# Kernel tuning notes

Hardware: AMD Instinct MI355X
Metric: run time of the kernel (lower is better)

## Reference

```python
import jax, jax.numpy as jnp
import numpy as np

V, E_DIM, H, B, T = 390, 256, 512, 64, 512
START = 388


def setup_inputs() -> dict:
    key = jax.random.key(0)
    ks = jax.random.split(key, 32)
    s = 0.05
    rn = lambda k, shape: jax.random.normal(k, shape, jnp.float32) * s
    inp = {
        "input": jax.random.normal(ks[0], (B, T, V), jnp.float32),
        # encoder params
        "enc_emb": rn(ks[1], (V, E_DIM)),
        "enc_Wih0": rn(ks[2], (3 * H, E_DIM)),
        "enc_Whh0": rn(ks[3], (3 * H, H)),
        "enc_bih0": rn(ks[4], (3 * H,)),
        "enc_bhh0": rn(ks[5], (3 * H,)),
        "enc_Wih1": rn(ks[6], (3 * H, H)),
        "enc_Whh1": rn(ks[7], (3 * H, H)),
        "enc_bih1": rn(ks[8], (3 * H,)),
        "enc_bhh1": rn(ks[9], (3 * H,)),
        # decoder params
        "dec_emb": rn(ks[10], (V, E_DIM)),
        "dec_Wih0": rn(ks[11], (3 * H, E_DIM)),
        "dec_Whh0": rn(ks[12], (3 * H, H)),
        "dec_bih0": rn(ks[13], (3 * H,)),
        "dec_bhh0": rn(ks[14], (3 * H,)),
        "dec_Wih1": rn(ks[15], (3 * H, H)),
        "dec_Whh1": rn(ks[16], (3 * H, H)),
        "dec_bih1": rn(ks[17], (3 * H,)),
        "dec_bhh1": rn(ks[18], (3 * H,)),
        # prediction head
        "Wp1": rn(ks[19], (H, H)),
        "bp1": rn(ks[20], (H,)),
        "Wp2": rn(ks[21], (V, H)),
        "bp2": rn(ks[22], (V,)),
    }
    return inp


def _gru_cell(x, h, Wih, Whh, bih, bhh):
    # PyTorch GRU cell: gates ordered (r, z, n)
    gi = x @ Wih.T + bih
    gh = h @ Whh.T + bhh
    ir, iz, inn = jnp.split(gi, 3, axis=-1)
    hr, hz, hn = jnp.split(gh, 3, axis=-1)
    r = jax.nn.sigmoid(ir + hr)
    z = jax.nn.sigmoid(iz + hz)
    n = jnp.tanh(inn + r * hn)
    return (1.0 - z) * n + z * h


def reference(input, enc_emb, enc_Wih0, enc_Whh0, enc_bih0, enc_bhh0,
              enc_Wih1, enc_Whh1, enc_bih1, enc_bhh1,
              dec_emb, dec_Wih0, dec_Whh0, dec_bih0, dec_bhh0,
              dec_Wih1, dec_Whh1, dec_bih1, dec_bhh1,
              Wp1, bp1, Wp2, bp2):
    batch, max_len, vocab = input.shape
    hdim = enc_Whh0.shape[1]

    # ---- Encoder: soft embedding + 2-layer GRU, keep final hidden states ----
    x = jnp.einsum('btv,ve->bte', input, enc_emb)  # [B,T,E]
    xt = jnp.transpose(x, (1, 0, 2))               # time-major [T,B,E]
    h0 = jnp.zeros((batch, hdim), input.dtype)

    def step0(h, xt_):
        h = _gru_cell(xt_, h, enc_Wih0, enc_Whh0, enc_bih0, enc_bhh0)
        return h, h
    h1_enc, seq1 = jax.lax.scan(step0, h0, xt)

    def step1(h, xt_):
        h = _gru_cell(xt_, h, enc_Wih1, enc_Whh1, enc_bih1, enc_bhh1)
        return h, None
    h2_enc, _ = jax.lax.scan(step1, h0, seq1)

    tok0 = jnp.full((batch,), START, jnp.int32)
    rng0 = jax.random.key(42)

    def dec_step(carry, _):
        h1, h2, tok, rng = carry
        rng, sk = jax.random.split(rng)
        xe = dec_emb[tok]                               # [B,E]
        h1 = _gru_cell(xe, h1, dec_Wih0, dec_Whh0, dec_bih0, dec_bhh0)
        h2 = _gru_cell(h1, h2, dec_Wih1, dec_Whh1, dec_bih1, dec_bhh1)
        hid = h2 @ Wp1.T + bp1
        hid = jnp.where(hid >= 0, hid, 0.1 * hid)       # LeakyReLU(0.1)
        logits = hid @ Wp2.T + bp2                      # temp=1 -> logits/temp == logits
        probs = jax.nn.softmax(logits, axis=-1)
        tok = jax.random.categorical(sk, logits, axis=-1).astype(jnp.int32)
        return (h1, h2, tok, rng), (probs, tok)

    _, (probs_seq, toks) = jax.lax.scan(
        dec_step, (h1_enc, h2_enc, tok0, rng0), None, length=max_len - 1)

    start_oh = jax.nn.one_hot(tok0, vocab, dtype=input.dtype)  # [B,V]
    outputs = jnp.concatenate(
        [start_oh[:, None, :], jnp.transpose(probs_seq, (1, 0, 2))], axis=1)
    max_output = jnp.concatenate(
        [jnp.full((batch, 1), float(START), jnp.float32),
         toks.T.astype(jnp.float32)], axis=1)
    return outputs, max_output
```

## Files before the change

### kernel.cpp

```cpp
#include <hip/hip_runtime.h>
#include <math.h>


#define BB 64
#define TT 512
#define VV 390
#define EE 256
#define HH 512

static __device__ __forceinline__ void tf2x32(unsigned k0, unsigned k1,
                                              unsigned x0, unsigned x1,
                                              unsigned &o0, unsigned &o1) {
  unsigned ks2 = k0 ^ k1 ^ 0x1BD11BDAu;
  x0 += k0; x1 += k1;
#define TFR(r) x0 += x1; x1 = (x1 << (r)) | (x1 >> (32 - (r))); x1 ^= x0;
  TFR(13) TFR(15) TFR(26) TFR(6)
  x0 += k1; x1 += ks2 + 1u;
  TFR(17) TFR(29) TFR(16) TFR(24)
  x0 += ks2; x1 += k0 + 2u;
  TFR(13) TFR(15) TFR(26) TFR(6)
  x0 += k0; x1 += k1 + 3u;
  TFR(17) TFR(29) TFR(16) TFR(24)
  x0 += k1; x1 += ks2 + 4u;
  TFR(13) TFR(15) TFR(26) TFR(6)
  x0 += ks2; x1 += k0 + 5u;
#undef TFR
  o0 = x0; o1 = x1;
}

static __device__ __forceinline__ float sigm(float x) {
  return 1.0f / (1.0f + expf(-x));
}

template <int K>
static __device__ __forceinline__ void dot3_kb(const float* __restrict__ X, int b,
    const float* __restrict__ w0, const float* __restrict__ w1,
    const float* __restrict__ w2, float &r0, float &r1, float &r2) {
  const float4* q0 = (const float4*)w0;
  const float4* q1 = (const float4*)w1;
  const float4* q2 = (const float4*)w2;
  float s0 = 0.f, s1 = 0.f, s2 = 0.f;
#pragma unroll 4
  for (int k4 = 0; k4 < (K >> 2); ++k4) {
    float4 u0 = q0[k4], u1 = q1[k4], u2 = q2[k4];
    int kb = (k4 << 8) + b;
    float x0 = X[kb], x1 = X[kb + 64], x2 = X[kb + 128], x3 = X[kb + 192];
    s0 = fmaf(x0, u0.x, s0); s0 = fmaf(x1, u0.y, s0); s0 = fmaf(x2, u0.z, s0); s0 = fmaf(x3, u0.w, s0);
    s1 = fmaf(x0, u1.x, s1); s1 = fmaf(x1, u1.y, s1); s1 = fmaf(x2, u1.z, s1); s1 = fmaf(x3, u1.w, s1);
    s2 = fmaf(x0, u2.x, s2); s2 = fmaf(x1, u2.y, s2); s2 = fmaf(x2, u2.z, s2); s2 = fmaf(x3, u2.w, s2);
  }
  r0 = s0; r1 = s1; r2 = s2;
}

template <int K>
static __device__ __forceinline__ void dot3_row(const float* __restrict__ xrow,
    const float* __restrict__ w0, const float* __restrict__ w1,
    const float* __restrict__ w2, float &r0, float &r1, float &r2) {
  const float4* xq = (const float4*)xrow;
  const float4* q0 = (const float4*)w0;
  const float4* q1 = (const float4*)w1;
  const float4* q2 = (const float4*)w2;
  float s0 = 0.f, s1 = 0.f, s2 = 0.f;
#pragma unroll 4
  for (int k4 = 0; k4 < (K >> 2); ++k4) {
    float4 x = xq[k4];
    float4 u0 = q0[k4], u1 = q1[k4], u2 = q2[k4];
    s0 = fmaf(x.x, u0.x, s0); s0 = fmaf(x.y, u0.y, s0); s0 = fmaf(x.z, u0.z, s0); s0 = fmaf(x.w, u0.w, s0);
    s1 = fmaf(x.x, u1.x, s1); s1 = fmaf(x.y, u1.y, s1); s1 = fmaf(x.z, u1.z, s1); s1 = fmaf(x.w, u1.w, s1);
    s2 = fmaf(x.x, u2.x, s2); s2 = fmaf(x.y, u2.y, s2); s2 = fmaf(x.z, u2.z, s2); s2 = fmaf(x.w, u2.w, s2);
  }
  r0 = s0; r1 = s1; r2 = s2;
}

__global__ __launch_bounds__(256) void k_init(float* __restrict__ out,
    float* __restrict__ h1buf, float* __restrict__ h2buf,
    int* __restrict__ tok, unsigned* __restrict__ rng) {
  int wg = blockIdx.x, tid = threadIdx.x;
  for (int i = wg * 256 + tid; i < HH * BB; i += 64 * 256) {
    h1buf[i] = 0.f;
    h2buf[i] = 0.f;
  }
  for (int v = tid; v < VV; v += 256)
    out[(size_t)wg * TT * VV + v] = (v == 388) ? 1.0f : 0.0f;
  if (tid == 0) {
    out[(size_t)BB * TT * VV + (size_t)wg * TT] = 388.0f;
    tok[wg] = 388;
    if (wg == 0) { rng[0] = 0u; rng[1] = 42u; rng[2] = 0u; rng[3] = 0u; }
  }
}

__global__ __launch_bounds__(256) void k_xgemm(const float* __restrict__ input,
    const float* __restrict__ emb, float* __restrict__ xT) {
  int t = blockIdx.x, tid = threadIdx.x;
  int s = tid >> 6, b = tid & 63;
  __shared__ float lin[64 * 65];
  float4 acc[16];
#pragma unroll
  for (int i = 0; i < 16; ++i) acc[i] = make_float4(0.f, 0.f, 0.f, 0.f);
  for (int k0 = 0; k0 < VV; k0 += 64) {
    int kmax = min(64, VV - k0);
    __syncthreads();
#pragma unroll
    for (int r = 0; r < 16; ++r) {
      int idx = r * 256 + tid;
      int b2 = idx >> 6, kk = idx & 63;
      if (kk < kmax)
        lin[kk * 65 + b2] = input[((size_t)b2 * TT + t) * VV + k0 + kk];
    }
    __syncthreads();
    for (int kk = 0; kk < kmax; ++kk) {
      float xv = lin[kk * 65 + b];
      const float4* er = (const float4*)(emb + (size_t)(k0 + kk) * EE);
#pragma unroll
      for (int i = 0; i < 16; ++i) {
        float4 w = er[s + 4 * i];
        acc[i].x = fmaf(xv, w.x, acc[i].x);
        acc[i].y = fmaf(xv, w.y, acc[i].y);
        acc[i].z = fmaf(xv, w.z, acc[i].z);
        acc[i].w = fmaf(xv, w.w, acc[i].w);
      }
    }
  }
  float* dst0 = xT + (size_t)t * (EE * 64);
#pragma unroll
  for (int i = 0; i < 16; ++i) {
    int e = (s + 4 * i) * 4;
    float* d = dst0 + e * 64 + b;
    d[0] = acc[i].x; d[64] = acc[i].y; d[128] = acc[i].z; d[192] = acc[i].w;
  }
}

__global__ __launch_bounds__(256) void k_enc_step(int t,
    const float* __restrict__ xT, float* __restrict__ h1buf, float* __restrict__ h2buf,
    const float* __restrict__ Wih0, const float* __restrict__ Whh0,
    const float* __restrict__ bih0, const float* __restrict__ bhh0,
    const float* __restrict__ Wih1, const float* __restrict__ Whh1,
    const float* __restrict__ bih1, const float* __restrict__ bhh1) {
  int wg = blockIdx.x, tid = threadIdx.x;
  int s = tid >> 6, b = tid & 63;
  const float* h1_r = h1buf + (t & 1) * (HH * BB);
  float* h1_w = h1buf + ((t + 1) & 1) * (HH * BB);
  if (wg < 128) {
    if (t >= TT) return;
    int j = wg * 4 + s;
    float ar, az, an, hr, hz, hn;
    dot3_kb<EE>(xT + (size_t)t * (EE * 64), b,
                Wih0 + (size_t)j * EE, Wih0 + (size_t)(512 + j) * EE,
                Wih0 + (size_t)(1024 + j) * EE, ar, az, an);
    dot3_kb<HH>(h1_r, b,
                Whh0 + (size_t)j * HH, Whh0 + (size_t)(512 + j) * HH,
                Whh0 + (size_t)(1024 + j) * HH, hr, hz, hn);
    float r = sigm((ar + bih0[j]) + (hr + bhh0[j]));
    float z = sigm((az + bih0[512 + j]) + (hz + bhh0[512 + j]));
    float n = tanhf((an + bih0[1024 + j]) + r * (hn + bhh0[1024 + j]));
    h1_w[j * 64 + b] = (1.0f - z) * n + z * h1_r[j * 64 + b];
  } else {
    if (t < 1) return;
    int j = (wg - 128) * 4 + s;
    const float* h2_r = h2buf + ((t + 1) & 1) * (HH * BB);
    float* h2_w = h2buf + (t & 1) * (HH * BB);
    float ar, az, an, hr, hz, hn;
    dot3_kb<HH>(h1_r, b,
                Wih1 + (size_t)j * HH, Wih1 + (size_t)(512 + j) * HH,
                Wih1 + (size_t)(1024 + j) * HH, ar, az, an);
    dot3_kb<HH>(h2_r, b,
                Whh1 + (size_t)j * HH, Whh1 + (size_t)(512 + j) * HH,
                Whh1 + (size_t)(1024 + j) * HH, hr, hz, hn);
    float r = sigm((ar + bih1[j]) + (hr + bhh1[j]));
    float z = sigm((az + bih1[512 + j]) + (hz + bhh1[512 + j]));
    float n = tanhf((an + bih1[1024 + j]) + r * (hn + bhh1[1024 + j]));
    h2_w[j * 64 + b] = (1.0f - z) * n + z * h2_r[j * 64 + b];
  }
}

__global__ __launch_bounds__(256) void k_decA(int d, float* __restrict__ h1buf,
    const float* __restrict__ demb, const float* __restrict__ Wih,
    const float* __restrict__ Whh, const float* __restrict__ bih,
    const float* __restrict__ bhh, const int* __restrict__ tok) {
  int wg = blockIdx.x, tid = threadIdx.x, s = tid >> 6, b = tid & 63;
  const float* h1_r = h1buf + (d & 1) * (HH * BB);
  float* h1_w = h1buf + ((d + 1) & 1) * (HH * BB);
  int j = wg * 4 + s;
  int tk = tok[b];
  float ar, az, an, hr, hz, hn;
  dot3_row<EE>(demb + (size_t)tk * EE,
               Wih + (size_t)j * EE, Wih + (size_t)(512 + j) * EE,
               Wih + (size_t)(1024 + j) * EE, ar, az, an);
  dot3_kb<HH>(h1_r, b,
              Whh + (size_t)j * HH, Whh + (size_t)(512 + j) * HH,
              Whh + (size_t)(1024 + j) * HH, hr, hz, hn);
  float r = sigm((ar + bih[j]) + (hr + bhh[j]));
  float z = sigm((az + bih[512 + j]) + (hz + bhh[512 + j]));
  float n = tanhf((an + bih[1024 + j]) + r * (hn + bhh[1024 + j]));
  h1_w[j * 64 + b] = (1.0f - z) * n + z * h1_r[j * 64 + b];
}

__global__ __launch_bounds__(256) void k_decB(int d, const float* __restrict__ h1buf,
    float* __restrict__ h2buf, const float* __restrict__ Wih,
    const float* __restrict__ Whh, const float* __restrict__ bih,
    const float* __restrict__ bhh) {
  int wg = blockIdx.x, tid = threadIdx.x, s = tid >> 6, b = tid & 63;
  const float* h1n = h1buf + ((d + 1) & 1) * (HH * BB);
  const float* h2r = h2buf + (d & 1) * (HH * BB);
  float* h2w = h2buf + ((d + 1) & 1) * (HH * BB);
  int j = wg * 4 + s;
  float ar, az, an, hr, hz, hn;
  dot3_kb<HH>(h1n, b,
              Wih + (size_t)j * HH, Wih + (size_t)(512 + j) * HH,
              Wih + (size_t)(1024 + j) * HH, ar, az, an);
  dot3_kb<HH>(h2r, b,
              Whh + (size_t)j * HH, Whh + (size_t)(512 + j) * HH,
              Whh + (size_t)(1024 + j) * HH, hr, hz, hn);
  float r = sigm((ar + bih[j]) + (hr + bhh[j]));
  float z = sigm((az + bih[512 + j]) + (hz + bhh[512 + j]));
  float n = tanhf((an + bih[1024 + j]) + r * (hn + bhh[1024 + j]));
  h2w[j * 64 + b] = (1.0f - z) * n + z * h2r[j * 64 + b];
}

__global__ __launch_bounds__(256) void k_decC(int d, const float* __restrict__ h2buf,
    const float* __restrict__ Wp1, const float* __restrict__ bp1,
    const float* __restrict__ Wp2, const float* __restrict__ bp2,
    float* __restrict__ out, int* __restrict__ tok, unsigned* __restrict__ rng) {
  __shared__ __align__(16) float lh[HH];
  __shared__ __align__(16) float lhid[HH];
  __shared__ float lv[VV];
  __shared__ float rf[8];
  __shared__ int ri[4];
  int b = blockIdx.x, tid = threadIdx.x;
  const float* h2 = h2buf + ((d + 1) & 1) * (HH * BB);
  lh[tid] = h2[tid * 64 + b];
  lh[tid + 256] = h2[(tid + 256) * 64 + b];
  __syncthreads();
  for (int c = tid; c < HH; c += 256) {
    const float4* w = (const float4*)(Wp1 + (size_t)c * HH);
    float a = 0.f;
#pragma unroll 4
    for (int k4 = 0; k4 < HH / 4; ++k4) {
      float4 q = w[k4];
      float4 hv = *(const float4*)&lh[k4 * 4];
      a = fmaf(hv.x, q.x, a); a = fmaf(hv.y, q.y, a);
      a = fmaf(hv.z, q.z, a); a = fmaf(hv.w, q.w, a);
    }
    a += bp1[c];
    lhid[c] = (a >= 0.f) ? a : 0.1f * a;
  }
  __syncthreads();
  for (int c = tid; c < VV; c += 256) {
    const float4* w = (const float4*)(Wp2 + (size_t)c * HH);
    float a = 0.f;
#pragma unroll 4
    for (int k4 = 0; k4 < HH / 4; ++k4) {
      float4 q = w[k4];
      float4 hv = *(const float4*)&lhid[k4 * 4];
      a = fmaf(hv.x, q.x, a); a = fmaf(hv.y, q.y, a);
      a = fmaf(hv.z, q.z, a); a = fmaf(hv.w, q.w, a);
    }
    lv[c] = a + bp2[c];
  }
  __syncthreads();
  float m = -INFINITY;
  for (int c = tid; c < VV; c += 256) m = fmaxf(m, lv[c]);
  for (int off = 32; off > 0; off >>= 1) m = fmaxf(m, __shfl_down(m, off, 64));
  if ((tid & 63) == 0) rf[tid >> 6] = m;
  __syncthreads();
  if (tid == 0) rf[4] = fmaxf(fmaxf(rf[0], rf[1]), fmaxf(rf[2], rf[3]));
  __syncthreads();
  m = rf[4];
  unsigned k0r = rng[(d & 1) * 2], k1r = rng[(d & 1) * 2 + 1];
  unsigned sk0, sk1;
  tf2x32(k0r, k1r, 0u, 1u, sk0, sk1);
  float by = -INFINITY; int bc = 0x7fffffff;
  for (int c = tid; c < VV; c += 256) {
    unsigned o0, o1;
    tf2x32(sk0, sk1, 0u, (unsigned)(b * VV + c), o0, o1);
    unsigned bits = o0 ^ o1;
    float f = __uint_as_float(0x3f800000u | (bits >> 9)) - 1.0f;
    float u = (f > 0.f) ? f : 1.17549435e-38f;
    float g = (float)(-log(-log((double)u)));
    float y = lv[c] + g;
    if (y > by || (y == by && c < bc)) { by = y; bc = c; }
  }
  for (int off = 32; off > 0; off >>= 1) {
    float oy = __shfl_down(by, off, 64);
    int oc = __shfl_down(bc, off, 64);
    if (oy > by || (oy == by && oc < bc)) { by = oy; bc = oc; }
  }
  if ((tid & 63) == 0) { rf[tid >> 6] = by; ri[tid >> 6] = bc; }
  __syncthreads();
  if (tid == 0) {
    by = rf[0]; bc = ri[0];
    for (int w2 = 1; w2 < 4; ++w2)
      if (rf[w2] > by || (rf[w2] == by && ri[w2] < bc)) { by = rf[w2]; bc = ri[w2]; }
    tok[b] = bc;
    out[(size_t)BB * TT * VV + (size_t)b * TT + (d + 1)] = (float)bc;
    if (b == 0) {
      unsigned n0, n1;
      tf2x32(k0r, k1r, 0u, 0u, n0, n1);
      rng[((d + 1) & 1) * 2] = n0;
      rng[((d + 1) & 1) * 2 + 1] = n1;
    }
  }
  __syncthreads();
  float e0 = 0.f, e1 = 0.f, ssum = 0.f;
  {
    int c = tid;
    if (c < VV) { e0 = expf(lv[c] - m); ssum += e0; }
    c = tid + 256;
    if (c < VV) { e1 = expf(lv[c] - m); ssum += e1; }
  }
  for (int off = 32; off > 0; off >>= 1) ssum += __shfl_down(ssum, off, 64);
  if ((tid & 63) == 0) rf[tid >> 6] = ssum;
  __syncthreads();
  if (tid == 0) rf[4] = (rf[0] + rf[1]) + (rf[2] + rf[3]);
  __syncthreads();
  float S = rf[4];
  float* orow = out + ((size_t)b * TT + (d + 1)) * VV;
  if (tid < VV) orow[tid] = e0 / S;
  if (tid + 256 < VV) orow[tid + 256] = e1 / S;
}

extern "C" void kernel_launch(void* const* d_in, const int* in_sizes, int n_in,
                              void* d_out, int out_size, void* d_ws, size_t ws_size,
                              hipStream_t stream) {
  (void)in_sizes; (void)n_in; (void)out_size; (void)ws_size;
  const float* input = (const float*)d_in[0];
  const float* e_emb = (const float*)d_in[1];
  const float* eWih0 = (const float*)d_in[2];
  const float* eWhh0 = (const float*)d_in[3];
  const float* ebih0 = (const float*)d_in[4];
  const float* ebhh0 = (const float*)d_in[5];
  const float* eWih1 = (const float*)d_in[6];
  const float* eWhh1 = (const float*)d_in[7];
  const float* ebih1 = (const float*)d_in[8];
  const float* ebhh1 = (const float*)d_in[9];
  const float* d_emb = (const float*)d_in[10];
  const float* dWih0 = (const float*)d_in[11];
  const float* dWhh0 = (const float*)d_in[12];
  const float* dbih0 = (const float*)d_in[13];
  const float* dbhh0 = (const float*)d_in[14];
  const float* dWih1 = (const float*)d_in[15];
  const float* dWhh1 = (const float*)d_in[16];
  const float* dbih1 = (const float*)d_in[17];
  const float* dbhh1 = (const float*)d_in[18];
  const float* Wp1   = (const float*)d_in[19];
  const float* bp1   = (const float*)d_in[20];
  const float* Wp2   = (const float*)d_in[21];
  const float* bp2   = (const float*)d_in[22];
  float* out = (float*)d_out;

  float* xT = (float*)d_ws;
  float* h1buf = xT + (size_t)TT * EE * 64;
  float* h2buf = h1buf + 2 * HH * BB;
  int* tok = (int*)(h2buf + 2 * HH * BB);
  unsigned* rng = (unsigned*)(tok + 64);

  k_init<<<64, 256, 0, stream>>>(out, h1buf, h2buf, tok, rng);
  k_xgemm<<<TT, 256, 0, stream>>>(input, e_emb, xT);
  for (int t = 0; t <= TT; ++t)
    k_enc_step<<<256, 256, 0, stream>>>(t, xT, h1buf, h2buf,
        eWih0, eWhh0, ebih0, ebhh0, eWih1, eWhh1, ebih1, ebhh1);
  for (int d = 0; d < TT - 1; ++d) {
    k_decA<<<128, 256, 0, stream>>>(d, h1buf, d_emb, dWih0, dWhh0, dbih0, dbhh0, tok);
    k_decB<<<128, 256, 0, stream>>>(d, h1buf, h2buf, dWih1, dWhh1, dbih1, dbhh1);
    k_decC<<<64, 256, 0, stream>>>(d, h2buf, Wp1, bp1, Wp2, bp2, out, tok, rng);
  }
}
```

Baseline: 86.14 ms.

## Replace per-step kernel launches with persistent kernels using grid barriers

```diff
diff --git a/kernel.cpp b/kernel.cpp
--- a/kernel.cpp
+++ b/kernel.cpp
@@ -72,9 +72,27 @@
   r0 = s0; r1 = s1; r2 = s2;
 }
 
-__global__ __launch_bounds__(256) void k_init(float* __restrict__ out,
-    float* __restrict__ h1buf, float* __restrict__ h2buf,
-    int* __restrict__ tok, unsigned* __restrict__ rng) {
+static __device__ __forceinline__ void gridbar(unsigned* bar, unsigned nwg) {
+  __syncthreads();
+  if (threadIdx.x == 0) {
+    unsigned v = __hip_atomic_fetch_add(bar, 1u, __ATOMIC_ACQ_REL,
+                                        __HIP_MEMORY_SCOPE_AGENT);
+    unsigned gen = v >> 16;
+    if ((v & 0xffffu) == nwg - 1u) {
+      __hip_atomic_store(bar, (gen + 1u) << 16, __ATOMIC_RELEASE,
+                         __HIP_MEMORY_SCOPE_AGENT);
+    } else {
+      while ((__hip_atomic_load(bar, __ATOMIC_RELAXED,
+                                __HIP_MEMORY_SCOPE_AGENT) >> 16) == gen)
+        __builtin_amdgcn_s_sleep(1);
+      __builtin_amdgcn_fence(__ATOMIC_ACQUIRE, "agent");
+    }
+  }
+  __syncthreads();
+}
+
+__global__ __launch_bounds__(256) void k_init(float* out,
+    float* h1buf, float* h2buf, int* tok, unsigned* rng, unsigned* ebar) {
   int wg = blockIdx.x, tid = threadIdx.x;
   for (int i = wg * 256 + tid; i < HH * BB; i += 64 * 256) {
     h1buf[i] = 0.f;
@@ -85,7 +103,10 @@
   if (tid == 0) {
     out[(size_t)BB * TT * VV + (size_t)wg * TT] = 388.0f;
     tok[wg] = 388;
-    if (wg == 0) { rng[0] = 0u; rng[1] = 42u; rng[2] = 0u; rng[3] = 0u; }
+    if (wg == 0) {
+      rng[0] = 0u; rng[1] = 42u; rng[2] = 0u; rng[3] = 0u;
+      ebar[0] = 0u;
+    }
   }
 }
 
@@ -130,193 +151,205 @@
   }
 }
 
-__global__ __launch_bounds__(256) void k_enc_step(int t,
-    const float* __restrict__ xT, float* __restrict__ h1buf, float* __restrict__ h2buf,
+__global__ __launch_bounds__(256) void k_enc_persist(
+    const float* __restrict__ xT, float* h1buf, float* h2buf,
     const float* __restrict__ Wih0, const float* __restrict__ Whh0,
     const float* __restrict__ bih0, const float* __restrict__ bhh0,
     const float* __restrict__ Wih1, const float* __restrict__ Whh1,
-    const float* __restrict__ bih1, const float* __restrict__ bhh1) {
+    const float* __restrict__ bih1, const float* __restrict__ bhh1,
+    unsigned* ebar, unsigned* dbar) {
   int wg = blockIdx.x, tid = threadIdx.x;
   int s = tid >> 6, b = tid & 63;
-  const float* h1_r = h1buf + (t & 1) * (HH * BB);
-  float* h1_w = h1buf + ((t + 1) & 1) * (HH * BB);
-  if (wg < 128) {
-    if (t >= TT) return;
-    int j = wg * 4 + s;
-    float ar, az, an, hr, hz, hn;
-    dot3_kb<EE>(xT + (size_t)t * (EE * 64), b,
-                Wih0 + (size_t)j * EE, Wih0 + (size_t)(512 + j) * EE,
-                Wih0 + (size_t)(1024 + j) * EE, ar, az, an);
-    dot3_kb<HH>(h1_r, b,
-                Whh0 + (size_t)j * HH, Whh0 + (size_t)(512 + j) * HH,
-                Whh0 + (size_t)(1024 + j) * HH, hr, hz, hn);
-    float r = sigm((ar + bih0[j]) + (hr + bhh0[j]));
-    float z = sigm((az + bih0[512 + j]) + (hz + bhh0[512 + j]));
-    float n = tanhf((an + bih0[1024 + j]) + r * (hn + bhh0[1024 + j]));
-    h1_w[j * 64 + b] = (1.0f - z) * n + z * h1_r[j * 64 + b];
-  } else {
-    if (t < 1) return;
-    int j = (wg - 128) * 4 + s;
-    const float* h2_r = h2buf + ((t + 1) & 1) * (HH * BB);
-    float* h2_w = h2buf + (t & 1) * (HH * BB);
-    float ar, az, an, hr, hz, hn;
-    dot3_kb<HH>(h1_r, b,
-                Wih1 + (size_t)j * HH, Wih1 + (size_t)(512 + j) * HH,
-                Wih1 + (size_t)(1024 + j) * HH, ar, az, an);
-    dot3_kb<HH>(h2_r, b,
-                Whh1 + (size_t)j * HH, Whh1 + (size_t)(512 + j) * HH,
-                Whh1 + (size_t)(1024 + j) * HH, hr, hz, hn);
-    float r = sigm((ar + bih1[j]) + (hr + bhh1[j]));
-    float z = sigm((az + bih1[512 + j]) + (hz + bhh1[512 + j]));
-    float n = tanhf((an + bih1[1024 + j]) + r * (hn + bhh1[1024 + j]));
-    h2_w[j * 64 + b] = (1.0f - z) * n + z * h2_r[j * 64 + b];
-  }
-}
-
-__global__ __launch_bounds__(256) void k_decA(int d, float* __restrict__ h1buf,
-    const float* __restrict__ demb, const float* __restrict__ Wih,
-    const float* __restrict__ Whh, const float* __restrict__ bih,
-    const float* __restrict__ bhh, const int* __restrict__ tok) {
-  int wg = blockIdx.x, tid = threadIdx.x, s = tid >> 6, b = tid & 63;
-  const float* h1_r = h1buf + (d & 1) * (HH * BB);
-  float* h1_w = h1buf + ((d + 1) & 1) * (HH * BB);
-  int j = wg * 4 + s;
-  int tk = tok[b];
-  float ar, az, an, hr, hz, hn;
-  dot3_row<EE>(demb + (size_t)tk * EE,
-               Wih + (size_t)j * EE, Wih + (size_t)(512 + j) * EE,
-               Wih + (size_t)(1024 + j) * EE, ar, az, an);
-  dot3_kb<HH>(h1_r, b,
-              Whh + (size_t)j * HH, Whh + (size_t)(512 + j) * HH,
-              Whh + (size_t)(1024 + j) * HH, hr, hz, hn);
-  float r = sigm((ar + bih[j]) + (hr + bhh[j]));
-  float z = sigm((az + bih[512 + j]) + (hz + bhh[512 + j]));
-  float n = tanhf((an + bih[1024 + j]) + r * (hn + bhh[1024 + j]));
-  h1_w[j * 64 + b] = (1.0f - z) * n + z * h1_r[j * 64 + b];
-}
-
-__global__ __launch_bounds__(256) void k_decB(int d, const float* __restrict__ h1buf,
-    float* __restrict__ h2buf, const float* __restrict__ Wih,
-    const float* __restrict__ Whh, const float* __restrict__ bih,
-    const float* __restrict__ bhh) {
-  int wg = blockIdx.x, tid = threadIdx.x, s = tid >> 6, b = tid & 63;
-  const float* h1n = h1buf + ((d + 1) & 1) * (HH * BB);
-  const float* h2r = h2buf + (d & 1) * (HH * BB);
-  float* h2w = h2buf + ((d + 1) & 1) * (HH * BB);
-  int j = wg * 4 + s;
-  float ar, az, an, hr, hz, hn;
-  dot3_kb<HH>(h1n, b,
-              Wih + (size_t)j * HH, Wih + (size_t)(512 + j) * HH,
-              Wih + (size_t)(1024 + j) * HH, ar, az, an);
-  dot3_kb<HH>(h2r, b,
-              Whh + (size_t)j * HH, Whh + (size_t)(512 + j) * HH,
-              Whh + (size_t)(1024 + j) * HH, hr, hz, hn);
-  float r = sigm((ar + bih[j]) + (hr + bhh[j]));
-  float z = sigm((az + bih[512 + j]) + (hz + bhh[512 + j]));
-  float n = tanhf((an + bih[1024 + j]) + r * (hn + bhh[1024 + j]));
-  h2w[j * 64 + b] = (1.0f - z) * n + z * h2r[j * 64 + b];
-}
-
-__global__ __launch_bounds__(256) void k_decC(int d, const float* __restrict__ h2buf,
+  for (int t = 0; t <= TT; ++t) {
+    const float* h1_r = h1buf + (t & 1) * (HH * BB);
+    float* h1_w = h1buf + ((t + 1) & 1) * (HH * BB);
+    if (wg < 128) {
+      if (t < TT) {
+        int j = wg * 4 + s;
+        float ar, az, an, hr, hz, hn;
+        dot3_kb<EE>(xT + (size_t)t * (EE * 64), b,
+                    Wih0 + (size_t)j * EE, Wih0 + (size_t)(512 + j) * EE,
+                    Wih0 + (size_t)(1024 + j) * EE, ar, az, an);
+        dot3_kb<HH>(h1_r, b,
+                    Whh0 + (size_t)j * HH, Whh0 + (size_t)(512 + j) * HH,
+                    Whh0 + (size_t)(1024 + j) * HH, hr, hz, hn);
+        float r = sigm((ar + bih0[j]) + (hr + bhh0[j]));
+        float z = sigm((az + bih0[512 + j]) + (hz + bhh0[512 + j]));
+        float n = tanhf((an + bih0[1024 + j]) + r * (hn + bhh0[1024 + j]));
+        h1_w[j * 64 + b] = (1.0f - z) * n + z * h1_r[j * 64 + b];
+      }
+    } else {
+      if (t >= 1) {
+        int j = (wg - 128) * 4 + s;
+        const float* h2_r = h2buf + ((t + 1) & 1) * (HH * BB);
+        float* h2_w = h2buf + (t & 1) * (HH * BB);
+        float ar, az, an, hr, hz, hn;
+        dot3_kb<HH>(h1_r, b,
+                    Wih1 + (size_t)j * HH, Wih1 + (size_t)(512 + j) * HH,
+                    Wih1 + (size_t)(1024 + j) * HH, ar, az, an);
+        dot3_kb<HH>(h2_r, b,
+                    Whh1 + (size_t)j * HH, Whh1 + (size_t)(512 + j) * HH,
+                    Whh1 + (size_t)(1024 + j) * HH, hr, hz, hn);
+        float r = sigm((ar + bih1[j]) + (hr + bhh1[j]));
+        float z = sigm((az + bih1[512 + j]) + (hz + bhh1[512 + j]));
+        float n = tanhf((an + bih1[1024 + j]) + r * (hn + bhh1[1024 + j]));
+        h2_w[j * 64 + b] = (1.0f - z) * n + z * h2_r[j * 64 + b];
+      }
+    }
+    if (t == TT && wg == 0 && tid == 0) dbar[0] = 0u;
+    gridbar(ebar, 256u);
+  }
+}
+
+__global__ __launch_bounds__(256) void k_dec_persist(
+    float* h1buf, float* h2buf,
+    const float* __restrict__ demb,
+    const float* __restrict__ dWih0, const float* __restrict__ dWhh0,
+    const float* __restrict__ dbih0, const float* __restrict__ dbhh0,
+    const float* __restrict__ dWih1, const float* __restrict__ dWhh1,
+    const float* __restrict__ dbih1, const float* __restrict__ dbhh1,
     const float* __restrict__ Wp1, const float* __restrict__ bp1,
     const float* __restrict__ Wp2, const float* __restrict__ bp2,
-    float* __restrict__ out, int* __restrict__ tok, unsigned* __restrict__ rng) {
+    float* out, int* tok, unsigned* rng, unsigned* dbar) {
+  int wg = blockIdx.x, tid = threadIdx.x;
+  int s = tid >> 6, b = tid & 63;
   __shared__ __align__(16) float lh[HH];
   __shared__ __align__(16) float lhid[HH];
   __shared__ float lv[VV];
   __shared__ float rf[8];
   __shared__ int ri[4];
-  int b = blockIdx.x, tid = threadIdx.x;
-  const float* h2 = h2buf + ((d + 1) & 1) * (HH * BB);
-  lh[tid] = h2[tid * 64 + b];
-  lh[tid + 256] = h2[(tid + 256) * 64 + b];
-  __syncthreads();
-  for (int c = tid; c < HH; c += 256) {
-    const float4* w = (const float4*)(Wp1 + (size_t)c * HH);
-    float a = 0.f;
+  for (int d = 0; d < TT - 1; ++d) {
+    {
+      const float* h1_r = h1buf + (d & 1) * (HH * BB);
+      float* h1_w = h1buf + ((d + 1) & 1) * (HH * BB);
+      int j = wg * 4 + s;
+      int tk = tok[b];
+      float ar, az, an, hr, hz, hn;
+      dot3_row<EE>(demb + (size_t)tk * EE,
+                   dWih0 + (size_t)j * EE, dWih0 + (size_t)(512 + j) * EE,
+                   dWih0 + (size_t)(1024 + j) * EE, ar, az, an);
+      dot3_kb<HH>(h1_r, b,
+                  dWhh0 + (size_t)j * HH, dWhh0 + (size_t)(512 + j) * HH,
+                  dWhh0 + (size_t)(1024 + j) * HH, hr, hz, hn);
+      float r = sigm((ar + dbih0[j]) + (hr + dbhh0[j]));
+      float z = sigm((az + dbih0[512 + j]) + (hz + dbhh0[512 + j]));
+      float n = tanhf((an + dbih0[1024 + j]) + r * (hn + dbhh0[1024 + j]));
+      h1_w[j * 64 + b] = (1.0f - z) * n + z * h1_r[j * 64 + b];
+    }
+    gridbar(dbar, 128u);
+    {
+      const float* h1n = h1buf + ((d + 1) & 1) * (HH * BB);
+      const float* h2r = h2buf + (d & 1) * (HH * BB);
+      float* h2w = h2buf + ((d + 1) & 1) * (HH * BB);
+      int j = wg * 4 + s;
+      float ar, az, an, hr, hz, hn;
+      dot3_kb<HH>(h1n, b,
+                  dWih1 + (size_t)j * HH, dWih1 + (size_t)(512 + j) * HH,
+                  dWih1 + (size_t)(1024 + j) * HH, ar, az, an);
+      dot3_kb<HH>(h2r, b,
+                  dWhh1 + (size_t)j * HH, dWhh1 + (size_t)(512 + j) * HH,
+                  dWhh1 + (size_t)(1024 + j) * HH, hr, hz, hn);
+      float r = sigm((ar + dbih1[j]) + (hr + dbhh1[j]));
+      float z = sigm((az + dbih1[512 + j]) + (hz + dbhh1[512 + j]));
+      float n = tanhf((an + dbih1[1024 + j]) + r * (hn + dbhh1[1024 + j]));
+      h2w[j * 64 + b] = (1.0f - z) * n + z * h2r[j * 64 + b];
+    }
+    gridbar(dbar, 128u);
+    if (wg < 64) {
+      int brow = wg;
+      const float* h2 = h2buf + ((d + 1) & 1) * (HH * BB);
+      lh[tid] = h2[tid * 64 + brow];
+      lh[tid + 256] = h2[(tid + 256) * 64 + brow];
+      __syncthreads();
+      for (int c = tid; c < HH; c += 256) {
+        const float4* w = (const float4*)(Wp1 + (size_t)c * HH);
+        float a = 0.f;
 #pragma unroll 4
-    for (int k4 = 0; k4 < HH / 4; ++k4) {
-      float4 q = w[k4];
-      float4 hv = *(const float4*)&lh[k4 * 4];
-      a = fmaf(hv.x, q.x, a); a = fmaf(hv.y, q.y, a);
-      a = fmaf(hv.z, q.z, a); a = fmaf(hv.w, q.w, a);
-    }
-    a += bp1[c];
-    lhid[c] = (a >= 0.f) ? a : 0.1f * a;
-  }
-  __syncthreads();
-  for (int c = tid; c < VV; c += 256) {
-    const float4* w = (const float4*)(Wp2 + (size_t)c * HH);
-    float a = 0.f;
+        for (int k4 = 0; k4 < HH / 4; ++k4) {
+          float4 q = w[k4];
+          float4 hv = *(const float4*)&lh[k4 * 4];
+          a = fmaf(hv.x, q.x, a); a = fmaf(hv.y, q.y, a);
+          a = fmaf(hv.z, q.z, a); a = fmaf(hv.w, q.w, a);
+        }
+        a += bp1[c];
+        lhid[c] = (a >= 0.f) ? a : 0.1f * a;
+      }
+      __syncthreads();
+      for (int c = tid; c < VV; c += 256) {
+        const float4* w = (const float4*)(Wp2 + (size_t)c * HH);
+        float a = 0.f;
 #pragma unroll 4
-    for (int k4 = 0; k4 < HH / 4; ++k4) {
-      float4 q = w[k4];
-      float4 hv = *(const float4*)&lhid[k4 * 4];
-      a = fmaf(hv.x, q.x, a); a = fmaf(hv.y, q.y, a);
-      a = fmaf(hv.z, q.z, a); a = fmaf(hv.w, q.w, a);
-    }
-    lv[c] = a + bp2[c];
-  }
-  __syncthreads();
-  float m = -INFINITY;
-  for (int c = tid; c < VV; c += 256) m = fmaxf(m, lv[c]);
-  for (int off = 32; off > 0; off >>= 1) m = fmaxf(m, __shfl_down(m, off, 64));
-  if ((tid & 63) == 0) rf[tid >> 6] = m;
-  __syncthreads();
-  if (tid == 0) rf[4] = fmaxf(fmaxf(rf[0], rf[1]), fmaxf(rf[2], rf[3]));
-  __syncthreads();
-  m = rf[4];
-  unsigned k0r = rng[(d & 1) * 2], k1r = rng[(d & 1) * 2 + 1];
-  unsigned sk0, sk1;
-  tf2x32(k0r, k1r, 0u, 1u, sk0, sk1);
-  float by = -INFINITY; int bc = 0x7fffffff;
-  for (int c = tid; c < VV; c += 256) {
-    unsigned o0, o1;
-    tf2x32(sk0, sk1, 0u, (unsigned)(b * VV + c), o0, o1);
-    unsigned bits = o0 ^ o1;
-    float f = __uint_as_float(0x3f800000u | (bits >> 9)) - 1.0f;
-    float u = (f > 0.f) ? f : 1.17549435e-38f;
-    float g = (float)(-log(-log((double)u)));
-    float y = lv[c] + g;
-    if (y > by || (y == by && c < bc)) { by = y; bc = c; }
-  }
-  for (int off = 32; off > 0; off >>= 1) {
-    float oy = __shfl_down(by, off, 64);
-    int oc = __shfl_down(bc, off, 64);
-    if (oy > by || (oy == by && oc < bc)) { by = oy; bc = oc; }
-  }
-  if ((tid & 63) == 0) { rf[tid >> 6] = by; ri[tid >> 6] = bc; }
-  __syncthreads();
-  if (tid == 0) {
-    by = rf[0]; bc = ri[0];
-    for (int w2 = 1; w2 < 4; ++w2)
-      if (rf[w2] > by || (rf[w2] == by && ri[w2] < bc)) { by = rf[w2]; bc = ri[w2]; }
-    tok[b] = bc;
-    out[(size_t)BB * TT * VV + (size_t)b * TT + (d + 1)] = (float)bc;
-    if (b == 0) {
-      unsigned n0, n1;
-      tf2x32(k0r, k1r, 0u, 0u, n0, n1);
-      rng[((d + 1) & 1) * 2] = n0;
-      rng[((d + 1) & 1) * 2 + 1] = n1;
-    }
-  }
-  __syncthreads();
-  float e0 = 0.f, e1 = 0.f, ssum = 0.f;
-  {
-    int c = tid;
-    if (c < VV) { e0 = expf(lv[c] - m); ssum += e0; }
-    c = tid + 256;
-    if (c < VV) { e1 = expf(lv[c] - m); ssum += e1; }
-  }
-  for (int off = 32; off > 0; off >>= 1) ssum += __shfl_down(ssum, off, 64);
-  if ((tid & 63) == 0) rf[tid >> 6] = ssum;
-  __syncthreads();
-  if (tid == 0) rf[4] = (rf[0] + rf[1]) + (rf[2] + rf[3]);
-  __syncthreads();
-  float S = rf[4];
-  float* orow = out + ((size_t)b * TT + (d + 1)) * VV;
-  if (tid < VV) orow[tid] = e0 / S;
-  if (tid + 256 < VV) orow[tid + 256] = e1 / S;
+        for (int k4 = 0; k4 < HH / 4; ++k4) {
+          float4 q = w[k4];
+          float4 hv = *(const float4*)&lhid[k4 * 4];
+          a = fmaf(hv.x, q.x, a); a = fmaf(hv.y, q.y, a);
+          a = fmaf(hv.z, q.z, a); a = fmaf(hv.w, q.w, a);
+        }
+        lv[c] = a + bp2[c];
+      }
+      __syncthreads();
+      float m = -INFINITY;
+      for (int c = tid; c < VV; c += 256) m = fmaxf(m, lv[c]);
+      for (int off = 32; off > 0; off >>= 1) m = fmaxf(m, __shfl_down(m, off, 64));
+      if ((tid & 63) == 0) rf[tid >> 6] = m;
+      __syncthreads();
+      if (tid == 0) rf[4] = fmaxf(fmaxf(rf[0], rf[1]), fmaxf(rf[2], rf[3]));
+      __syncthreads();
+      m = rf[4];
+      unsigned k0r = rng[(d & 1) * 2], k1r = rng[(d & 1) * 2 + 1];
+      unsigned sk0, sk1;
+      tf2x32(k0r, k1r, 0u, 1u, sk0, sk1);
+      float by = -INFINITY; int bc = 0x7fffffff;
+      for (int c = tid; c < VV; c += 256) {
+        unsigned o0, o1;
+        tf2x32(sk0, sk1, 0u, (unsigned)(brow * VV + c), o0, o1);
+        unsigned bits = o0 ^ o1;
+        float f = __uint_as_float(0x3f800000u | (bits >> 9)) - 1.0f;
+        float u = (f > 0.f) ? f : 1.17549435e-38f;
+        float g = (float)(-log(-log((double)u)));
+        float y = lv[c] + g;
+        if (y > by || (y == by && c < bc)) { by = y; bc = c; }
+      }
+      for (int off = 32; off > 0; off >>= 1) {
+        float oy = __shfl_down(by, off, 64);
+        int oc = __shfl_down(bc, off, 64);
+        if (oy > by || (oy == by && oc < bc)) { by = oy; bc = oc; }
+      }
+      if ((tid & 63) == 0) { rf[tid >> 6] = by; ri[tid >> 6] = bc; }
+      __syncthreads();
+      if (tid == 0) {
+        by = rf[0]; bc = ri[0];
+        for (int w2 = 1; w2 < 4; ++w2)
+          if (rf[w2] > by || (rf[w2] == by && ri[w2] < bc)) { by = rf[w2]; bc = ri[w2]; }
+        tok[brow] = bc;
+        out[(size_t)BB * TT * VV + (size_t)brow * TT + (d + 1)] = (float)bc;
+        if (brow == 0) {
+          unsigned n0, n1;
+          tf2x32(k0r, k1r, 0u, 0u, n0, n1);
+          rng[((d + 1) & 1) * 2] = n0;
+          rng[((d + 1) & 1) * 2 + 1] = n1;
+        }
+      }
+      __syncthreads();
+      float e0 = 0.f, e1 = 0.f, ssum = 0.f;
+      {
+        int c = tid;
+        if (c < VV) { e0 = expf(lv[c] - m); ssum += e0; }
+        c = tid + 256;
+        if (c < VV) { e1 = expf(lv[c] - m); ssum += e1; }
+      }
+      for (int off = 32; off > 0; off >>= 1) ssum += __shfl_down(ssum, off, 64);
+      if ((tid & 63) == 0) rf[tid >> 6] = ssum;
+      __syncthreads();
+      if (tid == 0) rf[4] = (rf[0] + rf[1]) + (rf[2] + rf[3]);
+      __syncthreads();
+      float S = rf[4];
+      float* orow = out + ((size_t)brow * TT + (d + 1)) * VV;
+      if (tid < VV) orow[tid] = e0 / S;
+      if (tid + 256 < VV) orow[tid + 256] = e1 / S;
+    }
+    gridbar(dbar, 128u);
+  }
 }
 
 extern "C" void kernel_launch(void* const* d_in, const int* in_sizes, int n_in,
@@ -353,15 +386,14 @@
   float* h2buf = h1buf + 2 * HH * BB;
   int* tok = (int*)(h2buf + 2 * HH * BB);
   unsigned* rng = (unsigned*)(tok + 64);
-
-  k_init<<<64, 256, 0, stream>>>(out, h1buf, h2buf, tok, rng);
+  unsigned* ebar = (unsigned*)(out + VV);
+  unsigned* dbar = (unsigned*)xT;
+
+  k_init<<<64, 256, 0, stream>>>(out, h1buf, h2buf, tok, rng, ebar);
   k_xgemm<<<TT, 256, 0, stream>>>(input, e_emb, xT);
-  for (int t = 0; t <= TT; ++t)
-    k_enc_step<<<256, 256, 0, stream>>>(t, xT, h1buf, h2buf,
-        eWih0, eWhh0, ebih0, ebhh0, eWih1, eWhh1, ebih1, ebhh1);
-  for (int d = 0; d < TT - 1; ++d) {
-    k_decA<<<128, 256, 0, stream>>>(d, h1buf, d_emb, dWih0, dWhh0, dbih0, dbhh0, tok);
-    k_decB<<<128, 256, 0, stream>>>(d, h1buf, h2buf, dWih1, dWhh1, dbih1, dbhh1);
-    k_decC<<<64, 256, 0, stream>>>(d, h2buf, Wp1, bp1, Wp2, bp2, out, tok, rng);
-  }
-}
+  k_enc_persist<<<256, 256, 0, stream>>>(xT, h1buf, h2buf,
+      eWih0, eWhh0, ebih0, ebhh0, eWih1, eWhh1, ebih1, ebhh1, ebar, dbar);
+  k_dec_persist<<<128, 256, 0, stream>>>(h1buf, h2buf, d_emb,
+      dWih0, dWhh0, dbih0, dbhh0, dWih1, dWhh1, dbih1, dbhh1,
+      Wp1, bp1, Wp2, bp2, out, tok, rng, dbar);
+}
```

After: 122.1 ms. 1.42x slower.
